# Performance work log

Measured on AMD Instinct MI355X. Metric: run time of the kernel, lower is better.

The kernel has to match this reference:

```python
import jax, jax.numpy as jnp
import numpy as np

N, D, E = 16384, 2048, 64          # tokens, d_model, n_experts
G = 8                               # n_expert_group
TOP_K = 8                           # experts selected per token
TOP_K_GROUP = 4                     # groups selected per token


def setup_inputs() -> dict:
    key = jax.random.key(0)
    k1, k2 = jax.random.split(key)
    x = jax.random.normal(k1, (N, D), dtype=jnp.float32)
    W = jax.random.normal(k2, (E, D), dtype=jnp.float32) * 0.02  # Linear weight
    b = jnp.zeros((E,), dtype=jnp.float32)                        # Linear bias
    bias = jnp.zeros((1, E), dtype=jnp.float32)                   # aux-loss-free routing bias
    return {"x": x, "W": W, "b": b, "bias": bias}


def reference(x, W, b, bias):
    n = x.shape[0]
    # linear + sigmoid
    score2weights = jax.nn.sigmoid(x @ W.T + b)       # [N, E]
    score = score2weights + bias                      # routing score with bias
    # group view
    score_g = score.reshape(n, G, -1)                 # [N, G, E/G]
    w_g = score2weights.reshape(n, G, -1)
    # group score = sum of top min(2, top_k) expert scores within each group
    top2, _ = jax.lax.top_k(score_g, min(2, TOP_K))   # [N, G, 2]
    group_score = top2.sum(axis=-1)                   # [N, G]
    # select top groups, build group mask (scatter)
    _, gidx = jax.lax.top_k(group_score, TOP_K_GROUP) # [N, TOP_K_GROUP]
    mask = jnp.zeros((n, G), score.dtype).at[jnp.arange(n)[:, None], gidx].set(1.0)
    # mask out non-selected groups, flatten back to expert dim
    score_m = (score_g * mask[..., None]).reshape(n, -1)   # [N, E]
    w_m = (w_g * mask[..., None]).reshape(n, -1)
    # final per-token expert selection + weight gather
    _, idx = jax.lax.top_k(score_m, TOP_K)            # [N, TOP_K] int32
    weights = jnp.take_along_axis(w_m, idx, axis=1)   # [N, TOP_K]
    return weights, idx
```

## Files before the change

kernel.cpp:

```cpp
#include <hip/hip_runtime.h>
#include <math.h>

#define DIM   2048
#define NEXP  64
#define NGRP  8
#define GSIZE 8
#define TOPK  8
#define TOPKG 4

#define NKS   8
#define KSL   (DIM / NKS)
#define SMSTR 548

#define TAU_E 2e-5f
#define TAU_G 4e-5f
#define NEG_INF (-3.4e38f)
#define WLOFF  16
#define WT_OFF  (1 << 18)
#define WT2_OFF (3 << 18)
#define SG_OFF  (1 << 21)

typedef __attribute__((ext_vector_type(8)))  _Float16 f16x8;
typedef __attribute__((ext_vector_type(16))) float    f32x16;

#define SB() __builtin_amdgcn_sched_barrier(0)

__global__ __launch_bounds__(256) void prep_kernel(
    const float* __restrict__ W, unsigned short* __restrict__ Wf,
    float* __restrict__ Wt, int* __restrict__ wl)
{
    const int g = blockIdx.x * 256 + threadIdx.x;
    const int e = g >> 11, k = g & 2047;
    const float w = W[g];
    const _Float16 hi = (_Float16)w;
    const _Float16 lo = (_Float16)(w - (float)hi);
    const int n2 = e >> 5, lcol = e & 31;
    const int kc = k >> 4, khalf = (k >> 3) & 1, j = k & 7;
    const int lane = (khalf << 5) | lcol;
    Wf[((((0 * 2 + n2) * 128 + kc) << 6) + lane) * 8 + j] =
        __builtin_bit_cast(unsigned short, hi);
    Wf[((((1 * 2 + n2) * 128 + kc) << 6) + lane) * 8 + j] =
        __builtin_bit_cast(unsigned short, lo);
    Wt[(((k >> 2) * 64 + e) << 2) + (k & 3)] = w;
    if (g < WLOFF) wl[g] = 0;
}

__global__ __launch_bounds__(512, 2) void gemm_kernel(
    const float* __restrict__ x,
    const unsigned short* __restrict__ Wf,
    const float* __restrict__ b,
    const float* __restrict__ bias,
    float* __restrict__ sSg)
{
    __shared__ float sM[NKS * SMSTR];

    const int tid  = threadIdx.x;
    const int ks   = tid >> 6;
    const int lane = tid & 63;
    const int tok0 = blockIdx.x * 32;
    const int l31  = lane & 31, lh = lane >> 5;

    const float* xr = x + (size_t)(tok0 + l31) * DIM + ks * KSL + lh * 8;
    const f16x8* Wfv = (const f16x8*)Wf;

    f32x16 acc0, acc1;
#pragma unroll
    for (int z = 0; z < 16; ++z) { acc0[z] = 0.f; acc1[z] = 0.f; }

    f16x8  Bq[2][4];
    float4 Xq[2][2];

#define ISSUE(t) do {                                                         \
        const int kc_ = ks * 16 + (t);                                        \
        Bq[(t) & 1][0] = Wfv[((0 * 2 + 0) * 128 + kc_) * 64 + lane];          \
        Bq[(t) & 1][1] = Wfv[((0 * 2 + 1) * 128 + kc_) * 64 + lane];          \
        Bq[(t) & 1][2] = Wfv[((1 * 2 + 0) * 128 + kc_) * 64 + lane];          \
        Bq[(t) & 1][3] = Wfv[((1 * 2 + 1) * 128 + kc_) * 64 + lane];          \
        Xq[(t) & 1][0] = *(const float4*)(xr + 16 * (t));                     \
        Xq[(t) & 1][1] = *(const float4*)(xr + 16 * (t) + 4);                 \
    } while (0)

    ISSUE(0); SB();
    ISSUE(1); SB();

#pragma unroll
    for (int t = 0; t < 16; ++t) {
        {
            const float4 qa = Xq[t & 1][0], qb = Xq[t & 1][1];
            const float xv[8] = {qa.x, qa.y, qa.z, qa.w, qb.x, qb.y, qb.z, qb.w};
            f16x8 ah, al;
#pragma unroll
            for (int j = 0; j < 8; j += 2) {
                const auto h2 = __builtin_amdgcn_cvt_pkrtz(xv[j], xv[j + 1]);
                const auto l2 = __builtin_amdgcn_cvt_pkrtz(xv[j]     - (float)h2.x,
                                                           xv[j + 1] - (float)h2.y);
                ah[j] = h2.x; ah[j + 1] = h2.y;
                al[j] = l2.x; al[j + 1] = l2.y;
            }
            acc0 = __builtin_amdgcn_mfma_f32_32x32x16_f16(ah, Bq[t & 1][0], acc0, 0, 0, 0);
            acc0 = __builtin_amdgcn_mfma_f32_32x32x16_f16(ah, Bq[t & 1][2], acc0, 0, 0, 0);
            acc0 = __builtin_amdgcn_mfma_f32_32x32x16_f16(al, Bq[t & 1][0], acc0, 0, 0, 0);
            acc1 = __builtin_amdgcn_mfma_f32_32x32x16_f16(ah, Bq[t & 1][1], acc1, 0, 0, 0);
            acc1 = __builtin_amdgcn_mfma_f32_32x32x16_f16(ah, Bq[t & 1][3], acc1, 0, 0, 0);
            acc1 = __builtin_amdgcn_mfma_f32_32x32x16_f16(al, Bq[t & 1][1], acc1, 0, 0, 0);
        }
        SB();
        if (t + 2 < 16) { ISSUE(t + 2); SB(); }
    }
#undef ISSUE

#pragma unroll
    for (int r = 0; r < 4; ++r) {
#pragma unroll
        for (int jj = 0; jj < 4; ++jj) {
            const int t8 = jj + 4 * lh;
            sM[ks * SMSTR + t8 * 68 + l31]      = acc0[4 * r + jj];
            sM[ks * SMSTR + t8 * 68 + l31 + 32] = acc1[4 * r + jj];
        }
        __syncthreads();
        {
            const int row = tid >> 6;
            const int e   = tid & 63;
            float sum = 0.f;
#pragma unroll
            for (int s = 0; s < NKS; ++s)
                sum += sM[s * SMSTR + row * 68 + e];
            const float logit = sum + b[e];
            const float wv = 1.0f / (1.0f + expf(-logit));
            sSg[(size_t)(tok0 + 8 * r + row) * NEXP + e] = wv + bias[e];
        }
        __syncthreads();
    }
}

__global__ __launch_bounds__(256) void route_kernel(
    const float* __restrict__ sSg,
    const float* __restrict__ bias,
    float* __restrict__ out_w,
    float* __restrict__ out_i,
    int* __restrict__ wl)
{
    __shared__ float sT[128][65];

    const int tid  = threadIdx.x;
    const int tok0 = blockIdx.x * 128;

    const float4* S4 = (const float4*)sSg + (size_t)tok0 * (NEXP / 4);
#pragma unroll
    for (int q = 0; q < 8; ++q) {
        const int idx = q * 256 + tid;
        const int tk  = idx >> 4, c4 = idx & 15;
        const float4 v = S4[idx];
        sT[tk][c4 * 4 + 0] = v.x;
        sT[tk][c4 * 4 + 1] = v.y;
        sT[tk][c4 * 4 + 2] = v.z;
        sT[tk][c4 * 4 + 3] = v.w;
    }
    __syncthreads();

    if (tid < 128) {
        const int t = tid;

        float gs[NGRP];
#pragma unroll
        for (int g = 0; g < NGRP; ++g) {
            float m1 = NEG_INF, m2 = NEG_INF;
#pragma unroll
            for (int j = 0; j < GSIZE; ++j) {
                const float v = sT[t][g * GSIZE + j];
                if (v > m1) { m2 = m1; m1 = v; }
                else if (v > m2) { m2 = v; }
            }
            gs[g] = m1 + m2;
        }

        unsigned gmask = 0u;
        float g4val = NEG_INF;
        for (int rr = 0; rr < TOPKG; ++rr) {
            float best = NEG_INF; int bi = 0;
#pragma unroll
            for (int g = 0; g < NGRP; ++g) {
                const float v = ((gmask >> g) & 1u) ? NEG_INF : gs[g];
                if (v > best) { best = v; bi = g; }
            }
            gmask |= 1u << bi;
            g4val = best;
        }
        float m5 = NEG_INF;
#pragma unroll
        for (int g = 0; g < NGRP; ++g)
            if (!((gmask >> g) & 1u) && gs[g] > m5) m5 = gs[g];
        const float margin_g = g4val - m5;

        unsigned long long chosen = 0ull;
        const size_t obase = (size_t)(tok0 + t) * TOPK;
        float vals[TOPK + 1];
        for (int rr = 0; rr < TOPK + 1; ++rr) {
            float best = NEG_INF; int bi = 0;
            for (int e = 0; e < NEXP; ++e) {
                float v = ((gmask >> (e >> 3)) & 1u) ? sT[t][e] : 0.0f;
                if ((chosen >> e) & 1ull) v = NEG_INF;
                if (v > best) { best = v; bi = e; }
            }
            vals[rr] = best;
            if (rr < TOPK) {
                chosen |= 1ull << (unsigned)bi;
                out_w[obase + rr] = ((gmask >> (bi >> 3)) & 1u)
                                  ? (sT[t][bi] - bias[bi]) : 0.0f;
                out_i[obase + rr] = (float)bi;
            }
        }
        float margin_e = 1e30f;
#pragma unroll
        for (int rr = 0; rr < TOPK; ++rr) {
            const float d = vals[rr] - vals[rr + 1];
            if (d < margin_e) margin_e = d;
        }

        if (margin_g < TAU_G || margin_e < TAU_E) {
            const int slot = atomicAdd(wl, 1);
            wl[WLOFF + slot] = tok0 + t;
        }
    }
}

__global__ __launch_bounds__(256) void gate_fix_kernel(
    const float* __restrict__ x,
    const float* __restrict__ Wt,
    const float* __restrict__ b,
    const float* __restrict__ bias,
    float* __restrict__ out_w,
    float* __restrict__ out_i,
    const int* __restrict__ wl)
{
    const int count = wl[0];

    __shared__ float sS2[4][NEXP];
    __shared__ float sW2[4][NEXP];

    const int tid  = threadIdx.x;
    const int wv_  = tid >> 6;
    const int lane = tid & 63;
    const int gw   = blockIdx.x * 4 + wv_;

    const float4* Wt4 = (const float4*)Wt;

    for (int widx = gw; widx < count; widx += (int)gridDim.x * 4) {
        const int tok = wl[WLOFF + widx];
        const float4* xr4 = (const float4*)(x + (size_t)tok * DIM);

        double a0 = 0., a1 = 0., a2 = 0., a3 = 0.;
#pragma unroll 4
        for (int k4 = 0; k4 < DIM / 4; ++k4) {
            const float4 wt = Wt4[(size_t)k4 * 64 + lane];
            const float4 xv = xr4[k4];
            a0 = fma((double)xv.x, (double)wt.x, a0);
            a1 = fma((double)xv.y, (double)wt.y, a1);
            a2 = fma((double)xv.z, (double)wt.z, a2);
            a3 = fma((double)xv.w, (double)wt.w, a3);
        }
        const double logit = ((a0 + a1) + (a2 + a3)) + (double)b[lane];
        const float wvv = (float)(1.0 / (1.0 + exp(-logit)));
        sW2[wv_][lane] = wvv;
        sS2[wv_][lane] = wvv + bias[lane];
        asm volatile("s_waitcnt lgkmcnt(0)" ::: "memory");
        __builtin_amdgcn_wave_barrier();

        float gsv[NGRP];
#pragma unroll
        for (int g = 0; g < NGRP; ++g) {
            float m1 = NEG_INF, m2 = NEG_INF;
#pragma unroll
            for (int j = 0; j < GSIZE; ++j) {
                const float v = sS2[wv_][g * GSIZE + j];
                if (v > m1) { m2 = m1; m1 = v; }
                else if (v > m2) { m2 = v; }
            }
            gsv[g] = m1 + m2;
        }
        unsigned gmask = 0u;
        for (int rr = 0; rr < TOPKG; ++rr) {
            float best = NEG_INF; int bi = 0;
#pragma unroll
            for (int g = 0; g < NGRP; ++g) {
                const float v = ((gmask >> g) & 1u) ? NEG_INF : gsv[g];
                if (v > best) { best = v; bi = g; }
            }
            gmask |= 1u << bi;
        }
        unsigned long long chosen = 0ull;
        float rw[TOPK]; int ri[TOPK];
        for (int rr = 0; rr < TOPK; ++rr) {
            float best = NEG_INF; int bi = 0;
            for (int e2 = 0; e2 < NEXP; ++e2) {
                float v = ((gmask >> (e2 >> 3)) & 1u) ? sS2[wv_][e2] : 0.0f;
                if ((chosen >> e2) & 1ull) v = NEG_INF;
                if (v > best) { best = v; bi = e2; }
            }
            chosen |= 1ull << (unsigned)bi;
            rw[rr] = ((gmask >> (bi >> 3)) & 1u) ? sW2[wv_][bi] : 0.0f;
            ri[rr] = bi;
        }
        if (lane == 0) {
            const size_t obase = (size_t)tok * TOPK;
#pragma unroll
            for (int rr = 0; rr < TOPK; ++rr) {
                out_w[obase + rr] = rw[rr];
                out_i[obase + rr] = (float)ri[rr];
            }
        }
        __builtin_amdgcn_wave_barrier();
    }
}

extern "C" void kernel_launch(void* const* d_in, const int* in_sizes, int n_in,
                              void* d_out, int out_size, void* d_ws, size_t ws_size,
                              hipStream_t stream) {
    const float* x    = (const float*)d_in[0];
    const float* W    = (const float*)d_in[1];
    const float* b    = (const float*)d_in[2];
    const float* bias = (const float*)d_in[3];

    const int n = in_sizes[0] / DIM;
    float* out_w = (float*)d_out;
    float* out_i = out_w + (size_t)n * TOPK;
    int*   wl    = (int*)d_ws;
    unsigned short* Wf = (unsigned short*)((char*)d_ws + WT_OFF);
    float* Wt    = (float*)((char*)d_ws + WT2_OFF);
    float* sSg   = (float*)((char*)d_ws + SG_OFF);

    prep_kernel<<<dim3((NEXP * DIM) / 256), dim3(256), 0, stream>>>(W, Wf, Wt, wl);
    gemm_kernel<<<dim3(n / 32), dim3(512), 0, stream>>>(x, Wf, b, bias, sSg);
    route_kernel<<<dim3(n / 128), dim3(256), 0, stream>>>(
        sSg, bias, out_w, out_i, wl);
    gate_fix_kernel<<<dim3(256), dim3(256), 0, stream>>>(
        x, Wt, b, bias, out_w, out_i, wl);
}
```

Measured before the change: 308.8 us.

## Split fix-up dot product across four waves per token with shared-memory reduction

The fix-up kernel now assigns one token per block instead of one per wave. The four waves each take a quarter of the K dimension in fp64, and the partial sums are reduced through shared memory. Routing selection then runs on a single thread. This shortens the serial per-token dot-product latency when the worklist of near-tie tokens is small. The cost is block-wide barriers and fewer tokens in flight per block.

New measurement: 279.9 us. 9.4% less time.

```diff
diff --git a/kernel.cpp b/kernel.cpp
--- a/kernel.cpp
+++ b/kernel.cpp
@@ -235,23 +235,23 @@
 {
     const int count = wl[0];
 
-    __shared__ float sS2[4][NEXP];
-    __shared__ float sW2[4][NEXP];
+    __shared__ double sPart[4][NEXP];
+    __shared__ float  sS2[NEXP], sW2[NEXP];
 
     const int tid  = threadIdx.x;
     const int wv_  = tid >> 6;
     const int lane = tid & 63;
-    const int gw   = blockIdx.x * 4 + wv_;
 
     const float4* Wt4 = (const float4*)Wt;
 
-    for (int widx = gw; widx < count; widx += (int)gridDim.x * 4) {
+    for (int widx = blockIdx.x; widx < count; widx += (int)gridDim.x) {
         const int tok = wl[WLOFF + widx];
         const float4* xr4 = (const float4*)(x + (size_t)tok * DIM);
 
         double a0 = 0., a1 = 0., a2 = 0., a3 = 0.;
-#pragma unroll 4
-        for (int k4 = 0; k4 < DIM / 4; ++k4) {
+#pragma unroll 8
+        for (int q = 0; q < DIM / 16; ++q) {
+            const int k4 = wv_ * (DIM / 16) + q;
             const float4 wt = Wt4[(size_t)k4 * 64 + lane];
             const float4 xv = xr4[k4];
             a0 = fma((double)xv.x, (double)wt.x, a0);
@@ -259,57 +259,57 @@
             a2 = fma((double)xv.z, (double)wt.z, a2);
             a3 = fma((double)xv.w, (double)wt.w, a3);
         }
-        const double logit = ((a0 + a1) + (a2 + a3)) + (double)b[lane];
-        const float wvv = (float)(1.0 / (1.0 + exp(-logit)));
-        sW2[wv_][lane] = wvv;
-        sS2[wv_][lane] = wvv + bias[lane];
-        asm volatile("s_waitcnt lgkmcnt(0)" ::: "memory");
-        __builtin_amdgcn_wave_barrier();
-
-        float gsv[NGRP];
-#pragma unroll
-        for (int g = 0; g < NGRP; ++g) {
-            float m1 = NEG_INF, m2 = NEG_INF;
-#pragma unroll
-            for (int j = 0; j < GSIZE; ++j) {
-                const float v = sS2[wv_][g * GSIZE + j];
-                if (v > m1) { m2 = m1; m1 = v; }
-                else if (v > m2) { m2 = v; }
-            }
-            gsv[g] = m1 + m2;
-        }
-        unsigned gmask = 0u;
-        for (int rr = 0; rr < TOPKG; ++rr) {
-            float best = NEG_INF; int bi = 0;
+        sPart[wv_][lane] = (a0 + a1) + (a2 + a3);
+        __syncthreads();
+
+        if (tid < NEXP) {
+            const double logit = ((sPart[0][tid] + sPart[1][tid])
+                                + (sPart[2][tid] + sPart[3][tid]))
+                               + (double)b[tid];
+            const float wvv = (float)(1.0 / (1.0 + exp(-logit)));
+            sW2[tid] = wvv;
+            sS2[tid] = wvv + bias[tid];
+        }
+        __syncthreads();
+
+        if (tid == 0) {
+            float gsv[NGRP];
 #pragma unroll
             for (int g = 0; g < NGRP; ++g) {
-                const float v = ((gmask >> g) & 1u) ? NEG_INF : gsv[g];
-                if (v > best) { best = v; bi = g; }
-            }
-            gmask |= 1u << bi;
-        }
-        unsigned long long chosen = 0ull;
-        float rw[TOPK]; int ri[TOPK];
-        for (int rr = 0; rr < TOPK; ++rr) {
-            float best = NEG_INF; int bi = 0;
-            for (int e2 = 0; e2 < NEXP; ++e2) {
-                float v = ((gmask >> (e2 >> 3)) & 1u) ? sS2[wv_][e2] : 0.0f;
-                if ((chosen >> e2) & 1ull) v = NEG_INF;
-                if (v > best) { best = v; bi = e2; }
-            }
-            chosen |= 1ull << (unsigned)bi;
-            rw[rr] = ((gmask >> (bi >> 3)) & 1u) ? sW2[wv_][bi] : 0.0f;
-            ri[rr] = bi;
-        }
-        if (lane == 0) {
+                float m1 = NEG_INF, m2 = NEG_INF;
+#pragma unroll
+                for (int j = 0; j < GSIZE; ++j) {
+                    const float v = sS2[g * GSIZE + j];
+                    if (v > m1) { m2 = m1; m1 = v; }
+                    else if (v > m2) { m2 = v; }
+                }
+                gsv[g] = m1 + m2;
+            }
+            unsigned gmask = 0u;
+            for (int rr = 0; rr < TOPKG; ++rr) {
+                float best = NEG_INF; int bi = 0;
+#pragma unroll
+                for (int g = 0; g < NGRP; ++g) {
+                    const float v = ((gmask >> g) & 1u) ? NEG_INF : gsv[g];
+                    if (v > best) { best = v; bi = g; }
+                }
+                gmask |= 1u << bi;
+            }
+            unsigned long long chosen = 0ull;
             const size_t obase = (size_t)tok * TOPK;
-#pragma unroll
             for (int rr = 0; rr < TOPK; ++rr) {
-                out_w[obase + rr] = rw[rr];
-                out_i[obase + rr] = (float)ri[rr];
-            }
-        }
-        __builtin_amdgcn_wave_barrier();
+                float best = NEG_INF; int bi = 0;
+                for (int e2 = 0; e2 < NEXP; ++e2) {
+                    float v = ((gmask >> (e2 >> 3)) & 1u) ? sS2[e2] : 0.0f;
+                    if ((chosen >> e2) & 1ull) v = NEG_INF;
+                    if (v > best) { best = v; bi = e2; }
+                }
+                chosen |= 1ull << (unsigned)bi;
+                out_w[obase + rr] = ((gmask >> (bi >> 3)) & 1u) ? sW2[bi] : 0.0f;
+                out_i[obase + rr] = (float)bi;
+            }
+        }
+        __syncthreads();
     }
 }
 
```
